# Kernel tuning notes

Measured on AMD Instinct MI355X. Metric: run time of the kernel, lower is better.

The kernel has to match this reference:

```python
import jax, jax.numpy as jnp
import numpy as np

B, S, D, H = 2, 2048, 512, 8
DK = D // H


def setup_inputs() -> dict:
    key = jax.random.key(0)
    ks = jax.random.split(key, 7)
    scale = 1.0 / np.sqrt(D)
    return {
        "query": jax.random.normal(ks[0], (B, S, D), dtype=jnp.float32),
        "key": jax.random.normal(ks[1], (B, S, D), dtype=jnp.float32),
        "value": jax.random.normal(ks[2], (B, S, D), dtype=jnp.float32),
        "w_q": jax.random.normal(ks[3], (D, D), dtype=jnp.float32) * scale,
        "w_k": jax.random.normal(ks[4], (D, D), dtype=jnp.float32) * scale,
        "w_v": jax.random.normal(ks[5], (D, D), dtype=jnp.float32) * scale,
        "w_o": jax.random.normal(ks[6], (D, D), dtype=jnp.float32) * scale,
    }


def reference(query, key, value, w_q, w_k, w_v, w_o):
    # Linear projections (torch nn.Linear: x @ W.T), split into heads -> [b, h, s, dk]
    def proj(x, w):
        return (x @ w.T).reshape(B, -1, H, DK).transpose(0, 2, 1, 3)

    q = proj(query, w_q)
    k = proj(key, w_k)
    v = proj(value, w_v)

    # scaled dot-product attention (unfused, materializes [b,h,s,s] scores)
    scores = jnp.einsum("bhqd,bhkd->bhqk", q, k) / np.sqrt(DK)
    p_attn = jax.nn.softmax(scores, axis=-1)
    out = jnp.einsum("bhqk,bhkd->bhqd", p_attn, v)  # [b,h,s,dk]

    # merge heads and final projection
    out = out.transpose(0, 2, 1, 3).reshape(B, -1, D)
    out = out @ w_o.T
    return (out, p_attn)
```

## Files before the change

### kernel.cpp

```cpp
#include <hip/hip_runtime.h>
#include <hip/hip_bf16.h>
#include <cstdint>
#include <cstddef>

#define BB 2
#define SS 2048
#define DD 512
#define HH 8
#define DKK 64

typedef __attribute__((ext_vector_type(8))) short bf16x8;
typedef __attribute__((ext_vector_type(4))) float f32x4;

__device__ __forceinline__ unsigned short f2bf(float f) {
    union { float f; unsigned u; } v; v.f = f;
    unsigned u = v.u;
    return (unsigned short)((u + 0x7fffu + ((u >> 16) & 1u)) >> 16);
}
__device__ __forceinline__ unsigned pack2(float a, float b) {
    return (unsigned)f2bf(a) | ((unsigned)f2bf(b) << 16);
}

typedef const __attribute__((address_space(1))) unsigned int* gp_t;
typedef __attribute__((address_space(3))) unsigned int* lp_t;
__device__ __forceinline__ void gload_lds16(const void* g, void* l) {
    __builtin_amdgcn_global_load_lds((gp_t)g, (lp_t)l, 16, 0, 0);
}

__global__ __launch_bounds__(256) void k_cvt(
    const float* __restrict__ q, const float* __restrict__ k, const float* __restrict__ v,
    const float* __restrict__ wq, const float* __restrict__ wk, const float* __restrict__ wv,
    const float* __restrict__ wo, unsigned short* __restrict__ dst,
    unsigned short* __restrict__ dwo)
{
    const size_t NX = (size_t)BB * SS * DD;
    const size_t NW = (size_t)DD * DD;
    const int y = blockIdx.y;
    const float* src; unsigned short* d; int n;
    switch (y) {
        case 0: src = q;  d = dst;                 n = (int)NX; break;
        case 1: src = k;  d = dst + NX;            n = (int)NX; break;
        case 2: src = v;  d = dst + 2 * NX;        n = (int)NX; break;
        case 3: src = wq; d = dst + 3 * NX;        n = (int)NW; break;
        case 4: src = wk; d = dst + 3 * NX + NW;   n = (int)NW; break;
        case 5: src = wv; d = dst + 3 * NX + 2*NW; n = (int)NW; break;
        default: src = wo; d = dwo;                n = (int)NW; break;
    }
    int idx = (blockIdx.x * 256 + threadIdx.x) * 8;
    if (idx >= n) return;
    float4 a = *(const float4*)(src + idx);
    float4 b = *(const float4*)(src + idx + 4);
    *(uint4*)(d + idx) = make_uint4(pack2(a.x,a.y), pack2(a.z,a.w), pack2(b.x,b.y), pack2(b.z,b.w));
}

__device__ __forceinline__ void gemm64_core(
    const unsigned short* __restrict__ A, const unsigned short* __restrict__ W,
    unsigned short* smem, int bm, int bn, int tid, f32x4 acc[4])
{
    const int w = tid >> 6, lane = tid & 63, quad = lane >> 4, l15 = lane & 15;
    for (int k0 = 0; k0 < DD; k0 += 64) {
        #pragma unroll
        for (int r = 0; r < 2; ++r) {
            int flat = r * 256 + tid;
            int row = flat >> 3, c = flat & 7, cs = c ^ (row & 7);
            gload_lds16(A + (size_t)(bm * 64 + row) * DD + k0 + cs * 8, &smem[flat * 8]);
        }
        #pragma unroll
        for (int r = 0; r < 2; ++r) {
            int flat = r * 256 + tid;
            int row = flat >> 3, c = flat & 7, cs = c ^ (row & 7);
            gload_lds16(W + (size_t)(bn * 64 + row) * DD + k0 + cs * 8, &smem[4096 + flat * 8]);
        }
        __syncthreads();
        int mrow = w * 16 + l15;
        bf16x8 a0 = *(const bf16x8*)&smem[(mrow * 8 + (quad ^ (mrow & 7))) * 8];
        bf16x8 a1 = *(const bf16x8*)&smem[(mrow * 8 + ((quad + 4) ^ (mrow & 7))) * 8];
        #pragma unroll
        for (int nt = 0; nt < 4; ++nt) {
            int nrow = nt * 16 + l15;
            bf16x8 b0 = *(const bf16x8*)&smem[4096 + (nrow * 8 + (quad ^ (nrow & 7))) * 8];
            bf16x8 b1 = *(const bf16x8*)&smem[4096 + (nrow * 8 + ((quad + 4) ^ (nrow & 7))) * 8];
            acc[nt] = __builtin_amdgcn_mfma_f32_16x16x32_bf16(a0, b0, acc[nt], 0, 0, 0);
            acc[nt] = __builtin_amdgcn_mfma_f32_16x16x32_bf16(a1, b1, acc[nt], 0, 0, 0);
        }
        __syncthreads();
    }
}

__global__ __launch_bounds__(256) void k_gemm_qkv(
    const unsigned short* __restrict__ scratch,
    unsigned short* __restrict__ Qw, unsigned short* __restrict__ Kw,
    unsigned short* __restrict__ Vt)
{
    __shared__ unsigned short smem[8192];
    const size_t NX = (size_t)BB * SS * DD, NW = (size_t)DD * DD;
    const int z = blockIdx.z;
    const unsigned short* A = scratch + (size_t)z * NX;
    const unsigned short* W = scratch + 3 * NX + (size_t)z * NW;
    const int bm = blockIdx.x, bn = blockIdx.y;
    const int tid = threadIdx.x, w = tid >> 6, lane = tid & 63, quad = lane >> 4, l15 = lane & 15;

    f32x4 acc[4];
    #pragma unroll
    for (int i = 0; i < 4; ++i) acc[i] = (f32x4){0.f, 0.f, 0.f, 0.f};
    gemm64_core(A, W, smem, bm, bn, tid, acc);

    if (z != 2) {
        const float sc = (z == 0) ? 0.125f : 1.0f;
        unsigned short* dbf = (z == 0) ? Qw : Kw;
        #pragma unroll
        for (int nt = 0; nt < 4; ++nt) {
            int n = bn * 64 + nt * 16 + l15;
            int h = n >> 6, dk = n & 63;
            #pragma unroll
            for (int rg = 0; rg < 4; ++rg) {
                int m = bm * 64 + w * 16 + quad * 4 + rg;
                int b = m >> 11, s = m & (SS - 1);
                dbf[(((size_t)(b * HH + h) * SS + s) << 6) + dk] = f2bf(acc[nt][rg] * sc);
            }
        }
    } else {
        unsigned short* T = smem;
        #pragma unroll
        for (int nt = 0; nt < 4; ++nt)
            #pragma unroll
            for (int rg = 0; rg < 4; ++rg)
                T[(w * 16 + quad * 4 + rg) * 72 + nt * 16 + l15] = f2bf(acc[nt][rg]);
        __syncthreads();
        int n = tid >> 2, s0 = (tid & 3) * 16;
        int ng = bn * 64 + n, h = ng >> 6, dk = ng & 63;
        int mg = bm * 64 + s0, b = mg >> 11, s = mg & (SS - 1);
        unsigned vals[8];
        #pragma unroll
        for (int i = 0; i < 8; ++i)
            vals[i] = (unsigned)T[(s0 + 2*i) * 72 + n] | ((unsigned)T[(s0 + 2*i + 1) * 72 + n] << 16);
        unsigned short* dp = Vt + ((size_t)(b * HH + h) * DKK + dk) * SS + s;
        ((uint4*)dp)[0] = make_uint4(vals[0], vals[1], vals[2], vals[3]);
        ((uint4*)dp)[1] = make_uint4(vals[4], vals[5], vals[6], vals[7]);
    }
}

__global__ __launch_bounds__(256) void k_attn2(
    const unsigned short* __restrict__ Qw, const unsigned short* __restrict__ Kw,
    const unsigned short* __restrict__ Vt, unsigned short* __restrict__ AO,
    float* __restrict__ P)
{
    __shared__ unsigned short Pl[2][4][16][68];
    const int qt = blockIdx.x, bh = blockIdx.y;
    const int tid = threadIdx.x, w = tid >> 6, lane = tid & 63, quad = lane >> 4, l15 = lane & 15;

    const unsigned short* Qb = Qw + ((size_t)bh * SS + qt * 64 + w * 16) * DKK;
    const unsigned short* Kb = Kw + (size_t)bh * SS * DKK;
    const unsigned short* Vb = Vt + (size_t)bh * DKK * SS;

    bf16x8 qa0 = *(const bf16x8*)&Qb[l15 * DKK + quad * 8];
    bf16x8 qa1 = *(const bf16x8*)&Qb[l15 * DKK + 32 + quad * 8];

    f32x4 oacc[4];
    #pragma unroll
    for (int i = 0; i < 4; ++i) oacc[i] = (f32x4){0.f, 0.f, 0.f, 0.f};
    float lsum[4] = {0.f, 0.f, 0.f, 0.f};

    #pragma unroll 2
    for (int kt = 0; kt < SS / 64; ++kt) {
        const int buf = kt & 1;
        const unsigned short* Kt = Kb + (size_t)kt * 64 * DKK;
        f32x4 sa[4];
        #pragma unroll
        for (int i = 0; i < 4; ++i) sa[i] = (f32x4){0.f, 0.f, 0.f, 0.f};
        #pragma unroll
        for (int jt = 0; jt < 4; ++jt) {
            bf16x8 b0 = *(const bf16x8*)&Kt[(jt * 16 + l15) * DKK + quad * 8];
            bf16x8 b1 = *(const bf16x8*)&Kt[(jt * 16 + l15) * DKK + 32 + quad * 8];
            sa[jt] = __builtin_amdgcn_mfma_f32_16x16x32_bf16(qa0, b0, sa[jt], 0, 0, 0);
            sa[jt] = __builtin_amdgcn_mfma_f32_16x16x32_bf16(qa1, b1, sa[jt], 0, 0, 0);
        }
        float ev[4][4];
        #pragma unroll
        for (int jt = 0; jt < 4; ++jt)
            #pragma unroll
            for (int rg = 0; rg < 4; ++rg)
                ev[jt][rg] = __expf(sa[jt][rg]);
        #pragma unroll
        for (int rg = 0; rg < 4; ++rg) {
            float s = ev[0][rg] + ev[1][rg] + ev[2][rg] + ev[3][rg];
            s += __shfl_xor(s, 1);
            s += __shfl_xor(s, 2);
            s += __shfl_xor(s, 4);
            s += __shfl_xor(s, 8);
            lsum[rg] += s;
        }
        #pragma unroll
        for (int jt = 0; jt < 4; ++jt)
            #pragma unroll
            for (int rg = 0; rg < 4; ++rg)
                Pl[buf][w][quad * 4 + rg][jt * 16 + l15] = f2bf(ev[jt][rg]);
        bf16x8 pa0 = *(const bf16x8*)&Pl[buf][w][l15][quad * 8];
        bf16x8 pa1 = *(const bf16x8*)&Pl[buf][w][l15][32 + quad * 8];
        #pragma unroll
        for (int dt = 0; dt < 4; ++dt) {
            const unsigned short* Vp = Vb + (size_t)(dt * 16 + l15) * SS + kt * 64;
            bf16x8 v0 = *(const bf16x8*)&Vp[quad * 8];
            bf16x8 v1 = *(const bf16x8*)&Vp[32 + quad * 8];
            oacc[dt] = __builtin_amdgcn_mfma_f32_16x16x32_bf16(pa0, v0, oacc[dt], 0, 0, 0);
            oacc[dt] = __builtin_amdgcn_mfma_f32_16x16x32_bf16(pa1, v1, oacc[dt], 0, 0, 0);
        }
    }

    float linv[4];
    #pragma unroll
    for (int rg = 0; rg < 4; ++rg) linv[rg] = 1.0f / lsum[rg];

    const int b = bh >> 3, h = bh & 7;
    const int srow = qt * 64 + w * 16 + quad * 4;
    #pragma unroll
    for (int dt = 0; dt < 4; ++dt)
        #pragma unroll
        for (int rg = 0; rg < 4; ++rg)
            AO[((size_t)(b * SS + srow + rg) << 9) + h * 64 + dt * 16 + l15] =
                f2bf(oacc[dt][rg] * linv[rg]);

    float* Pb = P + (((size_t)bh * SS + srow) << 11);
    #pragma unroll 2
    for (int kt = 0; kt < SS / 64; ++kt) {
        const unsigned short* Kt = Kb + (size_t)kt * 64 * DKK;
        #pragma unroll
        for (int jt = 0; jt < 4; ++jt) {
            bf16x8 b0 = *(const bf16x8*)&Kt[(jt * 16 + l15) * DKK + quad * 8];
            bf16x8 b1 = *(const bf16x8*)&Kt[(jt * 16 + l15) * DKK + 32 + quad * 8];
            f32x4 sa = (f32x4){0.f, 0.f, 0.f, 0.f};
            sa = __builtin_amdgcn_mfma_f32_16x16x32_bf16(qa0, b0, sa, 0, 0, 0);
            sa = __builtin_amdgcn_mfma_f32_16x16x32_bf16(qa1, b1, sa, 0, 0, 0);
            #pragma unroll
            for (int rg = 0; rg < 4; ++rg)
                __builtin_nontemporal_store(__expf(sa[rg]) * linv[rg],
                    &Pb[((size_t)rg << 11) + kt * 64 + jt * 16 + l15]);
        }
    }
}

__global__ __launch_bounds__(256) void k_gemm_o(
    const unsigned short* __restrict__ A, const unsigned short* __restrict__ W,
    float* __restrict__ out)
{
    __shared__ unsigned short smem[8192];
    const int bm = blockIdx.x, bn = blockIdx.y;
    const int tid = threadIdx.x, w = tid >> 6, lane = tid & 63, quad = lane >> 4, l15 = lane & 15;
    f32x4 acc[4];
    #pragma unroll
    for (int i = 0; i < 4; ++i) acc[i] = (f32x4){0.f, 0.f, 0.f, 0.f};
    gemm64_core(A, W, smem, bm, bn, tid, acc);
    #pragma unroll
    for (int nt = 0; nt < 4; ++nt)
        #pragma unroll
        for (int rg = 0; rg < 4; ++rg)
            out[(size_t)(bm * 64 + w * 16 + quad * 4 + rg) * DD + bn * 64 + nt * 16 + l15] =
                acc[nt][rg];
}

extern "C" void kernel_launch(void* const* d_in, const int* in_sizes, int n_in,
                              void* d_out, int out_size, void* d_ws, size_t ws_size,
                              hipStream_t stream) {
    const float* q  = (const float*)d_in[0];
    const float* k  = (const float*)d_in[1];
    const float* v  = (const float*)d_in[2];
    const float* wq = (const float*)d_in[3];
    const float* wk = (const float*)d_in[4];
    const float* wv = (const float*)d_in[5];
    const float* wo = (const float*)d_in[6];

    float* out = (float*)d_out;
    float* P   = out + (size_t)BB * SS * DD;

    const size_t NX = (size_t)BB * SS * DD;
    const size_t NW = (size_t)DD * DD;

    unsigned short* scratch = (unsigned short*)P;

    unsigned short* Qw  = (unsigned short*)d_ws;
    unsigned short* Kw  = Qw + NX;
    unsigned short* Vt  = Kw + NX;
    unsigned short* AO  = Vt + NX;
    unsigned short* Wo2 = AO + NX;

    k_cvt<<<dim3(1024, 7), 256, 0, stream>>>(q, k, v, wq, wk, wv, wo, scratch, Wo2);
    k_gemm_qkv<<<dim3(64, 8, 3), 256, 0, stream>>>(scratch, Qw, Kw, Vt);
    k_attn2<<<dim3(SS / 64, BB * HH), 256, 0, stream>>>(Qw, Kw, Vt, AO, P);
    k_gemm_o<<<dim3(64, 8), 256, 0, stream>>>(AO, Wo2, out);
}
```

Before: 460.4 us.

## Split attention into LDS-pipelined pass and separate wide P-write kernel

The attention kernel now stages K and V tiles into LDS with double-buffered async global-to-LDS loads, XOR-swizzled to avoid bank conflicts. It also remaps blocks so that heads group per XCD, and raises wave priority around the MFMA sections. Writing the probability matrix moves into a new kernel with four times as many blocks. That kernel recomputes scores from a stored 1/rowsum and writes 16-byte vectorized nontemporal stores through an LDS transpose. The aim is to hide memory latency and raise store bandwidth for the large P output, at the cost of an extra launch and a second QK^T pass.

New measurement: 393.5 us. 14.5% less time.

```diff
diff --git a/kernel.cpp b/kernel.cpp
--- a/kernel.cpp
+++ b/kernel.cpp
@@ -26,6 +26,9 @@
 __device__ __forceinline__ void gload_lds16(const void* g, void* l) {
     __builtin_amdgcn_global_load_lds((gp_t)g, (lp_t)l, 16, 0, 0);
 }
+
+#define VM_WAIT4 asm volatile("s_waitcnt vmcnt(4)" ::: "memory")
+#define VM_WAIT0 asm volatile("s_waitcnt vmcnt(0)" ::: "memory")
 
 __global__ __launch_bounds__(256) void k_cvt(
     const float* __restrict__ q, const float* __restrict__ k, const float* __restrict__ v,
@@ -140,13 +143,19 @@
     }
 }
 
-__global__ __launch_bounds__(256) void k_attn2(
+__global__ __launch_bounds__(256) void k_attn(
     const unsigned short* __restrict__ Qw, const unsigned short* __restrict__ Kw,
     const unsigned short* __restrict__ Vt, unsigned short* __restrict__ AO,
-    float* __restrict__ P)
-{
+    float* __restrict__ Linv)
+{
+    __shared__ unsigned short Kl[2][4096];
+    __shared__ unsigned short Vl[2][4096];
     __shared__ unsigned short Pl[2][4][16][68];
-    const int qt = blockIdx.x, bh = blockIdx.y;
+
+    const int id = blockIdx.x;
+    const int xcd = id & 7, j = id >> 3;
+    const int bh = xcd * 2 + (j >> 5), qt = j & 31;
+
     const int tid = threadIdx.x, w = tid >> 6, lane = tid & 63, quad = lane >> 4, l15 = lane & 15;
 
     const unsigned short* Qb = Qw + ((size_t)bh * SS + qt * 64 + w * 16) * DKK;
@@ -161,20 +170,45 @@
     for (int i = 0; i < 4; ++i) oacc[i] = (f32x4){0.f, 0.f, 0.f, 0.f};
     float lsum[4] = {0.f, 0.f, 0.f, 0.f};
 
-    #pragma unroll 2
-    for (int kt = 0; kt < SS / 64; ++kt) {
-        const int buf = kt & 1;
-        const unsigned short* Kt = Kb + (size_t)kt * 64 * DKK;
+    auto stage = [&](int kt, int b) {
+        #pragma unroll
+        for (int r = 0; r < 2; ++r) {
+            int flat = r * 256 + tid;
+            int row = flat >> 3, c = flat & 7, cs = c ^ (row & 7);
+            gload_lds16(Kb + (size_t)(kt * 64 + row) * DKK + cs * 8, &Kl[b][flat * 8]);
+        }
+        #pragma unroll
+        for (int r = 0; r < 2; ++r) {
+            int flat = r * 256 + tid;
+            int row = flat >> 3, c = flat & 7, cs = c ^ (row & 7);
+            gload_lds16(Vb + (size_t)row * SS + kt * 64 + cs * 8, &Vl[b][flat * 8]);
+        }
+    };
+
+    stage(0, 0);
+    stage(1, 1);
+
+    const int NT = SS / 64;
+    for (int kt = 0; kt < NT; ++kt) {
+        if (kt < NT - 1) { VM_WAIT4; } else { VM_WAIT0; }
+        __builtin_amdgcn_s_barrier();
+        __builtin_amdgcn_sched_barrier(0);
+        const int b = kt & 1;
+
         f32x4 sa[4];
         #pragma unroll
         for (int i = 0; i < 4; ++i) sa[i] = (f32x4){0.f, 0.f, 0.f, 0.f};
+        __builtin_amdgcn_s_setprio(1);
         #pragma unroll
         for (int jt = 0; jt < 4; ++jt) {
-            bf16x8 b0 = *(const bf16x8*)&Kt[(jt * 16 + l15) * DKK + quad * 8];
-            bf16x8 b1 = *(const bf16x8*)&Kt[(jt * 16 + l15) * DKK + 32 + quad * 8];
+            int row = jt * 16 + l15;
+            bf16x8 b0 = *(const bf16x8*)&Kl[b][(row * 8 + (quad ^ (row & 7))) * 8];
+            bf16x8 b1 = *(const bf16x8*)&Kl[b][(row * 8 + ((quad + 4) ^ (row & 7))) * 8];
             sa[jt] = __builtin_amdgcn_mfma_f32_16x16x32_bf16(qa0, b0, sa[jt], 0, 0, 0);
             sa[jt] = __builtin_amdgcn_mfma_f32_16x16x32_bf16(qa1, b1, sa[jt], 0, 0, 0);
         }
+        __builtin_amdgcn_s_setprio(0);
+
         float ev[4][4];
         #pragma unroll
         for (int jt = 0; jt < 4; ++jt)
@@ -194,35 +228,69 @@
         for (int jt = 0; jt < 4; ++jt)
             #pragma unroll
             for (int rg = 0; rg < 4; ++rg)
-                Pl[buf][w][quad * 4 + rg][jt * 16 + l15] = f2bf(ev[jt][rg]);
-        bf16x8 pa0 = *(const bf16x8*)&Pl[buf][w][l15][quad * 8];
-        bf16x8 pa1 = *(const bf16x8*)&Pl[buf][w][l15][32 + quad * 8];
+                Pl[b][w][quad * 4 + rg][jt * 16 + l15] = f2bf(ev[jt][rg]);
+        bf16x8 pa0 = *(const bf16x8*)&Pl[b][w][l15][quad * 8];
+        bf16x8 pa1 = *(const bf16x8*)&Pl[b][w][l15][32 + quad * 8];
+
+        __builtin_amdgcn_s_setprio(1);
         #pragma unroll
         for (int dt = 0; dt < 4; ++dt) {
-            const unsigned short* Vp = Vb + (size_t)(dt * 16 + l15) * SS + kt * 64;
-            bf16x8 v0 = *(const bf16x8*)&Vp[quad * 8];
-            bf16x8 v1 = *(const bf16x8*)&Vp[32 + quad * 8];
+            int row = dt * 16 + l15;
+            bf16x8 v0 = *(const bf16x8*)&Vl[b][(row * 8 + (quad ^ (row & 7))) * 8];
+            bf16x8 v1 = *(const bf16x8*)&Vl[b][(row * 8 + ((quad + 4) ^ (row & 7))) * 8];
             oacc[dt] = __builtin_amdgcn_mfma_f32_16x16x32_bf16(pa0, v0, oacc[dt], 0, 0, 0);
             oacc[dt] = __builtin_amdgcn_mfma_f32_16x16x32_bf16(pa1, v1, oacc[dt], 0, 0, 0);
         }
+        __builtin_amdgcn_s_setprio(0);
+
+        __builtin_amdgcn_s_barrier();
+        if (kt + 2 < NT) stage(kt + 2, b);
     }
 
     float linv[4];
     #pragma unroll
     for (int rg = 0; rg < 4; ++rg) linv[rg] = 1.0f / lsum[rg];
 
-    const int b = bh >> 3, h = bh & 7;
+    const int b2 = bh >> 3, h = bh & 7;
     const int srow = qt * 64 + w * 16 + quad * 4;
     #pragma unroll
     for (int dt = 0; dt < 4; ++dt)
         #pragma unroll
         for (int rg = 0; rg < 4; ++rg)
-            AO[((size_t)(b * SS + srow + rg) << 9) + h * 64 + dt * 16 + l15] =
+            AO[((size_t)(b2 * SS + srow + rg) << 9) + h * 64 + dt * 16 + l15] =
                 f2bf(oacc[dt][rg] * linv[rg]);
 
-    float* Pb = P + (((size_t)bh * SS + srow) << 11);
-    #pragma unroll 2
-    for (int kt = 0; kt < SS / 64; ++kt) {
+    if (l15 == 0) {
+        #pragma unroll
+        for (int rg = 0; rg < 4; ++rg)
+            Linv[(size_t)bh * SS + srow + rg] = linv[rg];
+    }
+}
+
+__global__ __launch_bounds__(256) void k_pwrite(
+    const unsigned short* __restrict__ Qw, const unsigned short* __restrict__ Kw,
+    const float* __restrict__ Linv, float* __restrict__ P)
+{
+    __shared__ float Tl[4][16][68];
+    const int id = blockIdx.x;
+    const int xcd = id & 7, j = id >> 3;
+    const int bh = xcd * 2 + (j >> 7);
+    const int rem = j & 127, qt = rem >> 2, ks = rem & 3;
+    const int tid = threadIdx.x, w = tid >> 6, lane = tid & 63, quad = lane >> 4, l15 = lane & 15;
+
+    const unsigned short* Qb = Qw + ((size_t)bh * SS + qt * 64 + w * 16) * DKK;
+    bf16x8 qa0 = *(const bf16x8*)&Qb[l15 * DKK + quad * 8];
+    bf16x8 qa1 = *(const bf16x8*)&Qb[l15 * DKK + 32 + quad * 8];
+
+    float linv[4];
+    #pragma unroll
+    for (int rg = 0; rg < 4; ++rg)
+        linv[rg] = Linv[(size_t)bh * SS + qt * 64 + w * 16 + quad * 4 + rg];
+
+    const unsigned short* Kb = Kw + (size_t)bh * SS * DKK + (size_t)ks * 512 * DKK;
+    float* Pb = P + (((size_t)bh * SS + qt * 64 + w * 16) << 11) + ks * 512;
+
+    for (int kt = 0; kt < 8; ++kt) {
         const unsigned short* Kt = Kb + (size_t)kt * 64 * DKK;
         #pragma unroll
         for (int jt = 0; jt < 4; ++jt) {
@@ -233,8 +301,14 @@
             sa = __builtin_amdgcn_mfma_f32_16x16x32_bf16(qa1, b1, sa, 0, 0, 0);
             #pragma unroll
             for (int rg = 0; rg < 4; ++rg)
-                __builtin_nontemporal_store(__expf(sa[rg]) * linv[rg],
-                    &Pb[((size_t)rg << 11) + kt * 64 + jt * 16 + l15]);
+                Tl[w][quad * 4 + rg][jt * 16 + l15] = __expf(sa[rg]) * linv[rg];
+        }
+        #pragma unroll
+        for (int c = 0; c < 4; ++c) {
+            int row = c * 4 + quad;
+            f32x4 val = *(const f32x4*)&Tl[w][row][l15 * 4];
+            __builtin_nontemporal_store(val,
+                (f32x4*)(Pb + ((size_t)row << 11) + kt * 64 + l15 * 4));
         }
     }
 }
@@ -277,14 +351,16 @@
 
     unsigned short* scratch = (unsigned short*)P;
 
-    unsigned short* Qw  = (unsigned short*)d_ws;
-    unsigned short* Kw  = Qw + NX;
-    unsigned short* Vt  = Kw + NX;
-    unsigned short* AO  = Vt + NX;
-    unsigned short* Wo2 = AO + NX;
+    unsigned short* Qw   = (unsigned short*)d_ws;
+    unsigned short* Kw   = Qw + NX;
+    unsigned short* Vt   = Kw + NX;
+    unsigned short* AO   = Vt + NX;
+    unsigned short* Wo2  = AO + NX;
+    float*          Linv = (float*)(Wo2 + NW);
 
     k_cvt<<<dim3(1024, 7), 256, 0, stream>>>(q, k, v, wq, wk, wv, wo, scratch, Wo2);
     k_gemm_qkv<<<dim3(64, 8, 3), 256, 0, stream>>>(scratch, Qw, Kw, Vt);
-    k_attn2<<<dim3(SS / 64, BB * HH), 256, 0, stream>>>(Qw, Kw, Vt, AO, P);
+    k_attn<<<dim3(512), 256, 0, stream>>>(Qw, Kw, Vt, AO, Linv);
+    k_pwrite<<<dim3(2048), 256, 0, stream>>>(Qw, Kw, Linv, P);
     k_gemm_o<<<dim3(64, 8), 256, 0, stream>>>(AO, Wo2, out);
 }
```
